# Kernel optimization log

Measured on AMD Instinct MI355X. Metric: run time of the kernel, lower is better.

Reference implementation:

```python
import jax, jax.numpy as jnp
import numpy as np

B, T, E, H = 2, 1024, 1024, 16
HD = E // H
TEMP = 0.5


def setup_inputs() -> dict:
    key = jax.random.key(0)
    ks = jax.random.split(key, 20)
    d = {
        "query1": jax.random.normal(ks[0], (B, T, E), jnp.float32),
        "query2": jax.random.normal(ks[1], (B, T, E), jnp.float32),
        "key": jax.random.normal(ks[2], (B, T, E), jnp.float32),
        "value": jax.random.normal(ks[3], (B, T, E), jnp.float32),
    }
    s = 1.0 / np.sqrt(E)
    names = ["Wq", "Wq2", "Wq3", "Wk", "Wv", "Wo"]
    for i, n in enumerate(names):
        d[n] = jax.random.normal(ks[4 + i], (E, E), jnp.float32) * s
        d["b" + n[1:]] = jax.random.normal(ks[10 + i], (E,), jnp.float32) * 0.01
    return d


def _heads(x):
    # [B,T,E] -> [B,H,T,HD]
    b, t, _ = x.shape
    return x.reshape(b, t, H, HD).transpose(0, 2, 1, 3)


def reference(query1, query2, key, value,
              Wq, bq, Wq2, bq2, Wq3, bq3, Wk, bk, Wv, bv, Wo, bo):
    q = _heads(query1 @ Wq.T + bq)
    q2 = _heads(query2 @ Wq2.T + bq2)
    q3 = _heads(key @ Wq3.T + bq3)
    k = _heads(key @ Wk.T + bk)
    v = _heads(value @ Wv.T + bv)
    b, _, t, _ = q.shape
    scale = 1.0 / np.sqrt(HD)

    def global_attn(qx):
        s = jnp.einsum('bhtd,bhsd->bhts', qx, k) * scale  # [B,H,T,T]
        # global softmax over flattened T*T, temperature-scaled, times T
        a = jax.nn.softmax((s / TEMP).reshape(b, H, t * t), axis=-1)
        return a.reshape(b, H, t, t) * t

    a1 = global_attn(q)
    a2 = global_attn(q2)
    a3 = global_attn(q3)
    attn_out = jnp.einsum('bhts,bhsd->bthd', (a1 + a2 + a3) / 3.0, v)
    attn_out = attn_out.reshape(b, t, E)
    output = attn_out @ Wo.T + bo
    return output, a1
```

## Files before the change

kernel.cpp:

```cpp
#include <hip/hip_runtime.h>
#include <hip/hip_bf16.h>


#define B_ 2
#define T_ 1024
#define E_ 1024
#define H_ 16
#define HD_ 64
#define BH_ 32

#define CEXP 0.36067376022224085f

typedef float f32x4 __attribute__((ext_vector_type(4)));
typedef short bfrag __attribute__((ext_vector_type(8)));

__device__ __forceinline__ unsigned short f2b(float f) {
  unsigned int u = __float_as_uint(f);
  u += 0x7fffu + ((u >> 16) & 1u);
  return (unsigned short)(u >> 16);
}

__device__ __forceinline__ float fexp2(float x) {
  float r;
  asm("v_exp_f32 %0, %1" : "=v"(r) : "v"(x));
  return r;
}

__device__ __forceinline__ void gl_lds16(const unsigned short* g, unsigned short* l) {
  __builtin_amdgcn_global_load_lds(
      reinterpret_cast<const __attribute__((address_space(1))) unsigned int*>(
          reinterpret_cast<uintptr_t>(g)),
      reinterpret_cast<__attribute__((address_space(3))) unsigned int*>(
          reinterpret_cast<uintptr_t>(l)),
      16, 0, 0);
}

struct CvtArgs { const float* src[10]; unsigned short* dst[10]; int n[10]; };

__global__ __launch_bounds__(256) void cvt_kernel(CvtArgs a) {
  const int z = blockIdx.y;
  const float* __restrict__ s = a.src[z];
  unsigned short* __restrict__ d = a.dst[z];
  const int n = a.n[z];
  const int stride = gridDim.x * 256 * 4;
  for (int i = (blockIdx.x * 256 + threadIdx.x) * 4; i < n; i += stride) {
    float4 v = *(const float4*)(s + i);
    ushort4 o;
    o.x = f2b(v.x); o.y = f2b(v.y); o.z = f2b(v.z); o.w = f2b(v.w);
    if (z == 9) {
      const int row = i >> 10, k = i & 1023;
      *(ushort4*)(d + (size_t)row * 2048 + k) = o;
      *(ushort4*)(d + (size_t)row * 2048 + 1024 + k) = o;
    } else {
      *(ushort4*)(d + i) = o;
    }
  }
}

template <int KLEN>
__device__ __forceinline__ void mm128_core(const unsigned short* __restrict__ A,
                                           const unsigned short* __restrict__ W,
                                           int m0, int n0,
                                           unsigned short* As, unsigned short* Bs,
                                           f32x4 acc[4][4]) {
  const int tid  = threadIdx.x;
  const int lane = tid & 63, w = tid >> 6;
  const int lrow = lane & 15, quad = lane >> 4;
  const int wm = (w >> 1) * 64, wn = (w & 1) * 64;
  const int srow = tid >> 2, soff = (tid & 3) * 8;

  const unsigned short* Ar0 = A + (size_t)(m0 + srow) * KLEN + soff;
  const unsigned short* Ar1 = Ar0 + (size_t)64 * KLEN;
  const unsigned short* Br0 = W + (size_t)(n0 + srow) * KLEN + soff;
  const unsigned short* Br1 = Br0 + (size_t)64 * KLEN;
  unsigned short* Ad0 = As + tid * 8;
  unsigned short* Ad1 = As + 2048 + tid * 8;
  unsigned short* Bd0 = Bs + tid * 8;
  unsigned short* Bd1 = Bs + 2048 + tid * 8;

  for (int k0 = 0; k0 < KLEN; k0 += 32) {
    __syncthreads();
    gl_lds16(Ar0 + k0, Ad0);
    gl_lds16(Ar1 + k0, Ad1);
    gl_lds16(Br0 + k0, Bd0);
    gl_lds16(Br1 + k0, Bd1);
    __syncthreads();
    bfrag af[4], bf_[4];
#pragma unroll
    for (int mt = 0; mt < 4; mt++)
      af[mt] = *(const bfrag*)(As + (wm + mt * 16 + lrow) * 32 + quad * 8);
#pragma unroll
    for (int nt = 0; nt < 4; nt++)
      bf_[nt] = *(const bfrag*)(Bs + (wn + nt * 16 + lrow) * 32 + quad * 8);
#pragma unroll
    for (int mt = 0; mt < 4; mt++)
#pragma unroll
      for (int nt = 0; nt < 4; nt++)
        acc[mt][nt] = __builtin_amdgcn_mfma_f32_16x16x32_bf16(af[mt], bf_[nt], acc[mt][nt], 0, 0, 0);
  }
}

struct ProjArgs {
  const unsigned short* X[5];
  const unsigned short* W[5];
  const float* bias[5];
  unsigned short* dst[5];
};

__global__ __launch_bounds__(256) void proj_kernel(ProjArgs pa) {
  __shared__ unsigned short As[128 * 32];
  __shared__ unsigned short Bs[128 * 32];
  const int z = blockIdx.z;
  const int m0 = blockIdx.y * 128, n0 = blockIdx.x * 128;
  f32x4 acc[4][4];
#pragma unroll
  for (int mt = 0; mt < 4; mt++)
#pragma unroll
    for (int nt = 0; nt < 4; nt++) acc[mt][nt] = (f32x4)0.f;

  mm128_core<E_>(pa.X[z], pa.W[z], m0, n0, As, Bs, acc);

  const int tid = threadIdx.x, lane = tid & 63, w = tid >> 6;
  const int lrow = lane & 15, quad = lane >> 4;
  const int wm = (w >> 1) * 64, wn = (w & 1) * 64;
  const float* __restrict__ bias = pa.bias[z];
  unsigned short* __restrict__ dst = pa.dst[z];
  float bv[4];
#pragma unroll
  for (int nt = 0; nt < 4; nt++) bv[nt] = bias[n0 + wn + nt * 16 + lrow];
#pragma unroll
  for (int mt = 0; mt < 4; mt++)
#pragma unroll
    for (int nt = 0; nt < 4; nt++)
#pragma unroll
      for (int ii = 0; ii < 4; ii++) {
        const int m = m0 + wm + mt * 16 + quad * 4 + ii;
        const int n = n0 + wn + nt * 16 + lrow;
        const float v = acc[mt][nt][ii] + bv[nt];
        const int b = m >> 10, t = m & 1023, h = n >> 6, dd = n & 63;
        size_t idx;
        if (z == 4)
          idx = ((size_t)((b * H_ + h) * HD_ + dd)) * T_ + t;
        else
          idx = ((size_t)((b * H_ + h) * T_ + t)) * HD_ + dd;
        dst[idx] = f2b(v);
      }
}

__global__ __launch_bounds__(256) void attn_sums_kernel(
    const unsigned short* __restrict__ Q1, const unsigned short* __restrict__ Q2,
    const unsigned short* __restrict__ Q3, const unsigned short* __restrict__ Kh,
    float* __restrict__ sums) {
  const int flat = blockIdx.x + 8 * (blockIdx.y + 2 * blockIdx.z);
  const int swz  = (flat & 7) * 64 + (flat >> 3);
  const int bx   = swz & 7;
  const int shalf = (swz >> 3) & 1;
  const int bh   = swz >> 4;

  const int tid = threadIdx.x, lane = tid & 63, w = tid >> 6;
  const int lrow = lane & 15, quad = lane >> 4;
  const int tw = w >> 1, sw = w & 1;
  const int tb = bx * 128 + tw * 64;
  const int sbase = shalf * 512;
  const size_t base = (size_t)bh * T_ * HD_;
  const unsigned short* Qs[3] = {Q1 + base, Q2 + base, Q3 + base};
  const unsigned short* Kb = Kh + base;

  float ls[3][4];
#pragma unroll
  for (int i = 0; i < 3; i++)
#pragma unroll
    for (int ii = 0; ii < 4; ii++) ls[i][ii] = 0.f;

  for (int j = 0; j < 4; j++) {
    const int sb = sbase + j * 128 + sw * 64;
#pragma unroll
    for (int i = 0; i < 3; i++) {
      f32x4 acc[4][4];
#pragma unroll
      for (int mt = 0; mt < 4; mt++)
#pragma unroll
        for (int nt = 0; nt < 4; nt++) acc[mt][nt] = (f32x4)0.f;
#pragma unroll
      for (int kk = 0; kk < 2; kk++) {
        bfrag af[4], bf_[4];
#pragma unroll
        for (int mt = 0; mt < 4; mt++)
          af[mt] = *(const bfrag*)(Qs[i] + (size_t)(tb + mt * 16 + lrow) * HD_ + kk * 32 + quad * 8);
#pragma unroll
        for (int nt = 0; nt < 4; nt++)
          bf_[nt] = *(const bfrag*)(Kb + (size_t)(sb + nt * 16 + lrow) * HD_ + kk * 32 + quad * 8);
#pragma unroll
        for (int mt = 0; mt < 4; mt++)
#pragma unroll
          for (int nt = 0; nt < 4; nt++)
            acc[mt][nt] = __builtin_amdgcn_mfma_f32_16x16x32_bf16(af[mt], bf_[nt], acc[mt][nt], 0, 0, 0);
      }
#pragma unroll
      for (int mt = 0; mt < 4; mt++)
#pragma unroll
        for (int nt = 0; nt < 4; nt++)
#pragma unroll
          for (int ii = 0; ii < 4; ii++)
            ls[i][ii] += fexp2(acc[mt][nt][ii] * CEXP);
    }
  }
#pragma unroll
  for (int i = 0; i < 3; i++) {
    float v = (ls[i][0] + ls[i][1]) + (ls[i][2] + ls[i][3]);
    for (int off = 32; off > 0; off >>= 1) v += __shfl_down(v, off, 64);
    if (lane == 0) atomicAdd(&sums[i * BH_ + bh], v);
  }
}

__global__ __launch_bounds__(256) void attn_main_kernel(
    const unsigned short* __restrict__ Q1, const unsigned short* __restrict__ Q2,
    const unsigned short* __restrict__ Q3, const unsigned short* __restrict__ Kh,
    const unsigned short* __restrict__ Vt, const float* __restrict__ sums,
    float* __restrict__ a1out, unsigned short* __restrict__ attn2) {
  __shared__ unsigned short P[128 * 136];
  const int flat = blockIdx.x + 8 * (blockIdx.y + 2 * blockIdx.z);
  const int swz  = (flat & 7) * 64 + (flat >> 3);
  const int bx   = swz & 7;
  const int sh   = (swz >> 3) & 1;
  const int bh   = swz >> 4;

  const int tid = threadIdx.x, lane = tid & 63, w = tid >> 6;
  const int lrow = lane & 15, quad = lane >> 4;
  const int tw = w >> 1, sw = w & 1, dw = sw;
  const int b = bh >> 4, h = bh & 15;
  const int tb = bx * 128 + tw * 64;
  const size_t base = (size_t)bh * T_ * HD_;
  const unsigned short* Qs[3] = {Q1 + base, Q2 + base, Q3 + base};
  const unsigned short* Kb = Kh + base;
  const unsigned short* Vb = Vt + (size_t)bh * HD_ * T_;

  float r[3];
#pragma unroll
  for (int i = 0; i < 3; i++) r[i] = (float)T_ / (3.f * sums[i * BH_ + bh]);
  const float a1s = 3.f * r[0];

  f32x4 oacc[4][2];
#pragma unroll
  for (int mt = 0; mt < 4; mt++) { oacc[mt][0] = (f32x4)0.f; oacc[mt][1] = (f32x4)0.f; }

  for (int s0 = sh * 512; s0 < sh * 512 + 512; s0 += 128) {
    const int sb = s0 + sw * 64;
    f32x4 pc[4][4];
#pragma unroll
    for (int mt = 0; mt < 4; mt++)
#pragma unroll
      for (int nt = 0; nt < 4; nt++) pc[mt][nt] = (f32x4)0.f;

#pragma unroll
    for (int i = 0; i < 3; i++) {
      f32x4 acc[4][4];
#pragma unroll
      for (int mt = 0; mt < 4; mt++)
#pragma unroll
        for (int nt = 0; nt < 4; nt++) acc[mt][nt] = (f32x4)0.f;
#pragma unroll
      for (int kk = 0; kk < 2; kk++) {
        bfrag af[4], bf_[4];
#pragma unroll
        for (int mt = 0; mt < 4; mt++)
          af[mt] = *(const bfrag*)(Qs[i] + (size_t)(tb + mt * 16 + lrow) * HD_ + kk * 32 + quad * 8);
#pragma unroll
        for (int nt = 0; nt < 4; nt++)
          bf_[nt] = *(const bfrag*)(Kb + (size_t)(sb + nt * 16 + lrow) * HD_ + kk * 32 + quad * 8);
#pragma unroll
        for (int mt = 0; mt < 4; mt++)
#pragma unroll
          for (int nt = 0; nt < 4; nt++)
            acc[mt][nt] = __builtin_amdgcn_mfma_f32_16x16x32_bf16(af[mt], bf_[nt], acc[mt][nt], 0, 0, 0);
      }
      const float ri = r[i];
#pragma unroll
      for (int mt = 0; mt < 4; mt++)
#pragma unroll
        for (int nt = 0; nt < 4; nt++)
#pragma unroll
          for (int ii = 0; ii < 4; ii++) {
            const float e = fexp2(acc[mt][nt][ii] * CEXP);
            pc[mt][nt][ii] += ri * e;
            if (i == 0) {
              const int t = tb + mt * 16 + quad * 4 + ii;
              const int s = sb + nt * 16 + lrow;
              __builtin_nontemporal_store(e * a1s,
                  a1out + ((size_t)bh * T_ + t) * T_ + s);
            }
          }
    }
    __syncthreads();
#pragma unroll
    for (int mt = 0; mt < 4; mt++)
#pragma unroll
      for (int nt = 0; nt < 4; nt++)
#pragma unroll
        for (int ii = 0; ii < 4; ii++) {
          const int tl = tw * 64 + mt * 16 + quad * 4 + ii;
          const int sl = sw * 64 + nt * 16 + lrow;
          P[tl * 136 + sl] = f2b(pc[mt][nt][ii]);
        }
    __syncthreads();
#pragma unroll
    for (int kk = 0; kk < 4; kk++) {
      bfrag pf[4], vf[2];
#pragma unroll
      for (int mt = 0; mt < 4; mt++)
        pf[mt] = *(const bfrag*)(P + (tw * 64 + mt * 16 + lrow) * 136 + kk * 32 + quad * 8);
#pragma unroll
      for (int nt = 0; nt < 2; nt++)
        vf[nt] = *(const bfrag*)(Vb + (size_t)(dw * 32 + nt * 16 + lrow) * T_ + s0 + kk * 32 + quad * 8);
#pragma unroll
      for (int mt = 0; mt < 4; mt++)
#pragma unroll
        for (int nt = 0; nt < 2; nt++)
          oacc[mt][nt] = __builtin_amdgcn_mfma_f32_16x16x32_bf16(pf[mt], vf[nt], oacc[mt][nt], 0, 0, 0);
    }
  }
#pragma unroll
  for (int mt = 0; mt < 4; mt++)
#pragma unroll
    for (int nt = 0; nt < 2; nt++)
#pragma unroll
      for (int ii = 0; ii < 4; ii++) {
        const int t = tb + mt * 16 + quad * 4 + ii;
        const int dd = dw * 32 + nt * 16 + lrow;
        attn2[((size_t)(b * T_ + t)) * 2048 + sh * 1024 + h * HD_ + dd] =
            f2b(oacc[mt][nt][ii]);
      }
}

__global__ __launch_bounds__(256) void outproj_kernel(
    const unsigned short* __restrict__ A2, const unsigned short* __restrict__ W2,
    const float* __restrict__ bias, float* __restrict__ out) {
  __shared__ unsigned short As[128 * 32];
  __shared__ unsigned short Bs[128 * 32];
  const int m0 = blockIdx.y * 128, n0 = blockIdx.x * 128;
  f32x4 acc[4][4];
#pragma unroll
  for (int mt = 0; mt < 4; mt++)
#pragma unroll
    for (int nt = 0; nt < 4; nt++) acc[mt][nt] = (f32x4)0.f;

  mm128_core<2048>(A2, W2, m0, n0, As, Bs, acc);

  const int tid = threadIdx.x, lane = tid & 63, w = tid >> 6;
  const int lrow = lane & 15, quad = lane >> 4;
  const int wm = (w >> 1) * 64, wn = (w & 1) * 64;
  float bv[4];
#pragma unroll
  for (int nt = 0; nt < 4; nt++) bv[nt] = bias[n0 + wn + nt * 16 + lrow];
#pragma unroll
  for (int mt = 0; mt < 4; mt++)
#pragma unroll
    for (int nt = 0; nt < 4; nt++)
#pragma unroll
      for (int ii = 0; ii < 4; ii++) {
        const int m = m0 + wm + mt * 16 + quad * 4 + ii;
        const int n = n0 + wn + nt * 16 + lrow;
        out[(size_t)m * E_ + n] = acc[mt][nt][ii] + bv[nt];
      }
}

extern "C" void kernel_launch(void* const* d_in, const int* in_sizes, int n_in,
                              void* d_out, int out_size, void* d_ws, size_t ws_size,
                              hipStream_t stream) {
  const float* q1f  = (const float*)d_in[0];
  const float* q2f  = (const float*)d_in[1];
  const float* keyf = (const float*)d_in[2];
  const float* valf = (const float*)d_in[3];
  const float* Wq  = (const float*)d_in[4];  const float* bq  = (const float*)d_in[5];
  const float* Wq2 = (const float*)d_in[6];  const float* bq2 = (const float*)d_in[7];
  const float* Wq3 = (const float*)d_in[8];  const float* bq3 = (const float*)d_in[9];
  const float* Wk  = (const float*)d_in[10]; const float* bk  = (const float*)d_in[11];
  const float* Wv  = (const float*)d_in[12]; const float* bv  = (const float*)d_in[13];
  const float* Wo  = (const float*)d_in[14]; const float* bo  = (const float*)d_in[15];

  char* ws = (char*)d_ws;
  const size_t MB = 1024 * 1024;
  unsigned short* xq1  = (unsigned short*)(ws + 0 * MB);
  unsigned short* xq2  = (unsigned short*)(ws + 4 * MB);
  unsigned short* xkey = (unsigned short*)(ws + 8 * MB);
  unsigned short* xval = (unsigned short*)(ws + 12 * MB);
  unsigned short* wq   = (unsigned short*)(ws + 16 * MB);
  unsigned short* wq2  = (unsigned short*)(ws + 18 * MB);
  unsigned short* wq3  = (unsigned short*)(ws + 20 * MB);
  unsigned short* wk   = (unsigned short*)(ws + 22 * MB);
  unsigned short* wv   = (unsigned short*)(ws + 24 * MB);
  unsigned short* Qh1  = (unsigned short*)(ws + 28 * MB);
  unsigned short* Qh2  = (unsigned short*)(ws + 32 * MB);
  unsigned short* Qh3  = (unsigned short*)(ws + 36 * MB);
  unsigned short* Kh   = (unsigned short*)(ws + 40 * MB);
  unsigned short* Vt   = (unsigned short*)(ws + 44 * MB);
  unsigned short* attn2 = (unsigned short*)(ws + 48 * MB);
  unsigned short* wo2   = (unsigned short*)(ws + 56 * MB);
  float* sums           = (float*)(ws + 60 * MB);

  CvtArgs ca;
  const float* srcs[10] = {q1f, q2f, keyf, valf, Wq, Wq2, Wq3, Wk, Wv, Wo};
  unsigned short* dsts[10] = {xq1, xq2, xkey, xval, wq, wq2, wq3, wk, wv, wo2};
  for (int i = 0; i < 10; i++) { ca.src[i] = srcs[i]; ca.dst[i] = dsts[i]; ca.n[i] = (i < 4) ? 2097152 : 1048576; }
  cvt_kernel<<<dim3(2048, 10), 256, 0, stream>>>(ca);

  hipMemsetAsync(sums, 0, 3 * BH_ * sizeof(float), stream);

  ProjArgs pa;
  const unsigned short* Xs[5] = {xq1, xq2, xkey, xkey, xval};
  const unsigned short* Ws_[5] = {wq, wq2, wq3, wk, wv};
  const float* Bi[5] = {bq, bq2, bq3, bk, bv};
  unsigned short* Ds[5] = {Qh1, Qh2, Qh3, Kh, Vt};
  for (int i = 0; i < 5; i++) { pa.X[i] = Xs[i]; pa.W[i] = Ws_[i]; pa.bias[i] = Bi[i]; pa.dst[i] = Ds[i]; }
  proj_kernel<<<dim3(8, 16, 5), 256, 0, stream>>>(pa);

  attn_sums_kernel<<<dim3(8, 2, BH_), 256, 0, stream>>>(Qh1, Qh2, Qh3, Kh, sums);

  float* out = (float*)d_out;
  attn_main_kernel<<<dim3(8, 2, BH_), 256, 0, stream>>>(Qh1, Qh2, Qh3, Kh, Vt, sums,
                                                        out + 2097152, attn2);

  outproj_kernel<<<dim3(8, 16), 256, 0, stream>>>(attn2, wo2, bo, out);
}
```

Before: 391.2 us.

## Split attention main kernel per query branch, add combine kernel, reuse Q fragments

The attention main kernel now launches one block per query branch (3x grid) over the full key range instead of per key half. Each block computes one branch's probabilities and writes a partial output, and a new combine kernel sums the three bf16 partials. The out-projection then runs with K=1024 instead of the duplicated 2048 layout. The sums kernel splits keys into quarters, hoists Q fragments out of the key loop, and both kernels get occupancy launch bounds. This trades an extra pass over the partial outputs and an extra bf16 rounding for more parallelism and smaller per-block register state.

```diff
diff --git a/kernel.cpp b/kernel.cpp
--- a/kernel.cpp
+++ b/kernel.cpp
@@ -18,6 +18,10 @@
   unsigned int u = __float_as_uint(f);
   u += 0x7fffu + ((u >> 16) & 1u);
   return (unsigned short)(u >> 16);
+}
+
+__device__ __forceinline__ float b2f(unsigned short u) {
+  return __uint_as_float((unsigned int)u << 16);
 }
 
 __device__ __forceinline__ float fexp2(float x) {
@@ -47,13 +51,7 @@
     float4 v = *(const float4*)(s + i);
     ushort4 o;
     o.x = f2b(v.x); o.y = f2b(v.y); o.z = f2b(v.z); o.w = f2b(v.w);
-    if (z == 9) {
-      const int row = i >> 10, k = i & 1023;
-      *(ushort4*)(d + (size_t)row * 2048 + k) = o;
-      *(ushort4*)(d + (size_t)row * 2048 + 1024 + k) = o;
-    } else {
-      *(ushort4*)(d + i) = o;
-    }
+    *(ushort4*)(d + i) = o;
   }
 }
 
@@ -147,35 +145,40 @@
       }
 }
 
-__global__ __launch_bounds__(256) void attn_sums_kernel(
+__global__ __launch_bounds__(256, 4) void attn_sums_kernel(
     const unsigned short* __restrict__ Q1, const unsigned short* __restrict__ Q2,
     const unsigned short* __restrict__ Q3, const unsigned short* __restrict__ Kh,
     float* __restrict__ sums) {
-  const int flat = blockIdx.x + 8 * (blockIdx.y + 2 * blockIdx.z);
-  const int swz  = (flat & 7) * 64 + (flat >> 3);
+  const int flat = blockIdx.x + 8 * (blockIdx.y + 4 * blockIdx.z);
+  const int swz  = (flat & 7) * 128 + (flat >> 3);
   const int bx   = swz & 7;
-  const int shalf = (swz >> 3) & 1;
-  const int bh   = swz >> 4;
+  const int sy   = (swz >> 3) & 3;
+  const int bh   = swz >> 5;
 
   const int tid = threadIdx.x, lane = tid & 63, w = tid >> 6;
   const int lrow = lane & 15, quad = lane >> 4;
   const int tw = w >> 1, sw = w & 1;
   const int tb = bx * 128 + tw * 64;
-  const int sbase = shalf * 512;
+  const int sbase = sy * 256;
   const size_t base = (size_t)bh * T_ * HD_;
   const unsigned short* Qs[3] = {Q1 + base, Q2 + base, Q3 + base};
   const unsigned short* Kb = Kh + base;
 
-  float ls[3][4];
-#pragma unroll
-  for (int i = 0; i < 3; i++)
-#pragma unroll
-    for (int ii = 0; ii < 4; ii++) ls[i][ii] = 0.f;
-
-  for (int j = 0; j < 4; j++) {
-    const int sb = sbase + j * 128 + sw * 64;
-#pragma unroll
-    for (int i = 0; i < 3; i++) {
+  float ls[3][2];
+#pragma unroll
+  for (int i = 0; i < 3; i++) { ls[i][0] = 0.f; ls[i][1] = 0.f; }
+
+#pragma unroll
+  for (int i = 0; i < 3; i++) {
+    bfrag qf[2][4];
+#pragma unroll
+    for (int kk = 0; kk < 2; kk++)
+#pragma unroll
+      for (int mt = 0; mt < 4; mt++)
+        qf[kk][mt] = *(const bfrag*)(Qs[i] + (size_t)(tb + mt * 16 + lrow) * HD_ + kk * 32 + quad * 8);
+#pragma unroll
+    for (int j = 0; j < 2; j++) {
+      const int sb = sbase + j * 128 + sw * 64;
       f32x4 acc[4][4];
 #pragma unroll
       for (int mt = 0; mt < 4; mt++)
@@ -183,10 +186,7 @@
         for (int nt = 0; nt < 4; nt++) acc[mt][nt] = (f32x4)0.f;
 #pragma unroll
       for (int kk = 0; kk < 2; kk++) {
-        bfrag af[4], bf_[4];
-#pragma unroll
-        for (int mt = 0; mt < 4; mt++)
-          af[mt] = *(const bfrag*)(Qs[i] + (size_t)(tb + mt * 16 + lrow) * HD_ + kk * 32 + quad * 8);
+        bfrag bf_[4];
 #pragma unroll
         for (int nt = 0; nt < 4; nt++)
           bf_[nt] = *(const bfrag*)(Kb + (size_t)(sb + nt * 16 + lrow) * HD_ + kk * 32 + quad * 8);
@@ -194,7 +194,7 @@
         for (int mt = 0; mt < 4; mt++)
 #pragma unroll
           for (int nt = 0; nt < 4; nt++)
-            acc[mt][nt] = __builtin_amdgcn_mfma_f32_16x16x32_bf16(af[mt], bf_[nt], acc[mt][nt], 0, 0, 0);
+            acc[mt][nt] = __builtin_amdgcn_mfma_f32_16x16x32_bf16(qf[kk][mt], bf_[nt], acc[mt][nt], 0, 0, 0);
       }
 #pragma unroll
       for (int mt = 0; mt < 4; mt++)
@@ -202,28 +202,29 @@
         for (int nt = 0; nt < 4; nt++)
 #pragma unroll
           for (int ii = 0; ii < 4; ii++)
-            ls[i][ii] += fexp2(acc[mt][nt][ii] * CEXP);
+            ls[i][ii & 1] += fexp2(acc[mt][nt][ii] * CEXP);
     }
   }
 #pragma unroll
   for (int i = 0; i < 3; i++) {
-    float v = (ls[i][0] + ls[i][1]) + (ls[i][2] + ls[i][3]);
+    float v = ls[i][0] + ls[i][1];
     for (int off = 32; off > 0; off >>= 1) v += __shfl_down(v, off, 64);
     if (lane == 0) atomicAdd(&sums[i * BH_ + bh], v);
   }
 }
 
-__global__ __launch_bounds__(256) void attn_main_kernel(
+__global__ __launch_bounds__(256, 3) void attn_main_kernel(
     const unsigned short* __restrict__ Q1, const unsigned short* __restrict__ Q2,
     const unsigned short* __restrict__ Q3, const unsigned short* __restrict__ Kh,
     const unsigned short* __restrict__ Vt, const float* __restrict__ sums,
-    float* __restrict__ a1out, unsigned short* __restrict__ attn2) {
+    float* __restrict__ a1out, unsigned short* __restrict__ attnP) {
   __shared__ unsigned short P[128 * 136];
-  const int flat = blockIdx.x + 8 * (blockIdx.y + 2 * blockIdx.z);
-  const int swz  = (flat & 7) * 64 + (flat >> 3);
-  const int bx   = swz & 7;
-  const int sh   = (swz >> 3) & 1;
-  const int bh   = swz >> 4;
+  const int flat = blockIdx.x + 8 * (blockIdx.y + 3 * blockIdx.z);
+  const int swz  = (flat & 7) * 96 + (flat >> 3);
+  const int bh   = swz / 24;
+  const int rem  = swz % 24;
+  const int iq   = rem >> 3;
+  const int bx   = rem & 7;
 
   const int tid = threadIdx.x, lane = tid & 63, w = tid >> 6;
   const int lrow = lane & 15, quad = lane >> 4;
@@ -231,65 +232,43 @@
   const int b = bh >> 4, h = bh & 15;
   const int tb = bx * 128 + tw * 64;
   const size_t base = (size_t)bh * T_ * HD_;
-  const unsigned short* Qs[3] = {Q1 + base, Q2 + base, Q3 + base};
+  const unsigned short* Qb = (iq == 0 ? Q1 : (iq == 1 ? Q2 : Q3)) + base;
   const unsigned short* Kb = Kh + base;
   const unsigned short* Vb = Vt + (size_t)bh * HD_ * T_;
-
-  float r[3];
-#pragma unroll
-  for (int i = 0; i < 3; i++) r[i] = (float)T_ / (3.f * sums[i * BH_ + bh]);
-  const float a1s = 3.f * r[0];
+  unsigned short* __restrict__ dst = attnP + (size_t)iq * (2048 * 1024);
+
+  const float r = (float)T_ / (3.f * sums[iq * BH_ + bh]);
+  const float a1s = 3.f * r;
+
+  bfrag qf[2][4];
+#pragma unroll
+  for (int kk = 0; kk < 2; kk++)
+#pragma unroll
+    for (int mt = 0; mt < 4; mt++)
+      qf[kk][mt] = *(const bfrag*)(Qb + (size_t)(tb + mt * 16 + lrow) * HD_ + kk * 32 + quad * 8);
 
   f32x4 oacc[4][2];
 #pragma unroll
   for (int mt = 0; mt < 4; mt++) { oacc[mt][0] = (f32x4)0.f; oacc[mt][1] = (f32x4)0.f; }
 
-  for (int s0 = sh * 512; s0 < sh * 512 + 512; s0 += 128) {
+  for (int s0 = 0; s0 < T_; s0 += 128) {
     const int sb = s0 + sw * 64;
-    f32x4 pc[4][4];
+    f32x4 acc[4][4];
 #pragma unroll
     for (int mt = 0; mt < 4; mt++)
 #pragma unroll
-      for (int nt = 0; nt < 4; nt++) pc[mt][nt] = (f32x4)0.f;
-
-#pragma unroll
-    for (int i = 0; i < 3; i++) {
-      f32x4 acc[4][4];
-#pragma unroll
-      for (int mt = 0; mt < 4; mt++)
-#pragma unroll
-        for (int nt = 0; nt < 4; nt++) acc[mt][nt] = (f32x4)0.f;
-#pragma unroll
-      for (int kk = 0; kk < 2; kk++) {
-        bfrag af[4], bf_[4];
-#pragma unroll
-        for (int mt = 0; mt < 4; mt++)
-          af[mt] = *(const bfrag*)(Qs[i] + (size_t)(tb + mt * 16 + lrow) * HD_ + kk * 32 + quad * 8);
+      for (int nt = 0; nt < 4; nt++) acc[mt][nt] = (f32x4)0.f;
+#pragma unroll
+    for (int kk = 0; kk < 2; kk++) {
+      bfrag bf_[4];
+#pragma unroll
+      for (int nt = 0; nt < 4; nt++)
+        bf_[nt] = *(const bfrag*)(Kb + (size_t)(sb + nt * 16 + lrow) * HD_ + kk * 32 + quad * 8);
+#pragma unroll
+      for (int mt = 0; mt < 4; mt++)
 #pragma unroll
         for (int nt = 0; nt < 4; nt++)
-          bf_[nt] = *(const bfrag*)(Kb + (size_t)(sb + nt * 16 + lrow) * HD_ + kk * 32 + quad * 8);
-#pragma unroll
-        for (int mt = 0; mt < 4; mt++)
-#pragma unroll
-          for (int nt = 0; nt < 4; nt++)
-            acc[mt][nt] = __builtin_amdgcn_mfma_f32_16x16x32_bf16(af[mt], bf_[nt], acc[mt][nt], 0, 0, 0);
-      }
-      const float ri = r[i];
-#pragma unroll
-      for (int mt = 0; mt < 4; mt++)
-#pragma unroll
-        for (int nt = 0; nt < 4; nt++)
-#pragma unroll
-          for (int ii = 0; ii < 4; ii++) {
-            const float e = fexp2(acc[mt][nt][ii] * CEXP);
-            pc[mt][nt][ii] += ri * e;
-            if (i == 0) {
-              const int t = tb + mt * 16 + quad * 4 + ii;
-              const int s = sb + nt * 16 + lrow;
-              __builtin_nontemporal_store(e * a1s,
-                  a1out + ((size_t)bh * T_ + t) * T_ + s);
-            }
-          }
+          acc[mt][nt] = __builtin_amdgcn_mfma_f32_16x16x32_bf16(qf[kk][mt], bf_[nt], acc[mt][nt], 0, 0, 0);
     }
     __syncthreads();
 #pragma unroll
@@ -298,9 +277,14 @@
       for (int nt = 0; nt < 4; nt++)
 #pragma unroll
         for (int ii = 0; ii < 4; ii++) {
+          const float e = fexp2(acc[mt][nt][ii] * CEXP);
           const int tl = tw * 64 + mt * 16 + quad * 4 + ii;
           const int sl = sw * 64 + nt * 16 + lrow;
-          P[tl * 136 + sl] = f2b(pc[mt][nt][ii]);
+          P[tl * 136 + sl] = f2b(r * e);
+          if (iq == 0) {
+            __builtin_nontemporal_store(e * a1s,
+                a1out + ((size_t)bh * T_ + (tb - tw * 64 + tl)) * T_ + s0 + sl);
+          }
         }
     __syncthreads();
 #pragma unroll
@@ -327,13 +311,29 @@
       for (int ii = 0; ii < 4; ii++) {
         const int t = tb + mt * 16 + quad * 4 + ii;
         const int dd = dw * 32 + nt * 16 + lrow;
-        attn2[((size_t)(b * T_ + t)) * 2048 + sh * 1024 + h * HD_ + dd] =
-            f2b(oacc[mt][nt][ii]);
+        dst[((size_t)(b * T_ + t)) * E_ + h * HD_ + dd] = f2b(oacc[mt][nt][ii]);
       }
 }
 
+__global__ __launch_bounds__(256) void combine_kernel(
+    const unsigned short* __restrict__ p0, const unsigned short* __restrict__ p1,
+    const unsigned short* __restrict__ p2, unsigned short* __restrict__ dstc) {
+  const size_t i = ((size_t)blockIdx.x * 256 + threadIdx.x) * 8;
+  bfrag a = *(const bfrag*)(p0 + i);
+  bfrag b = *(const bfrag*)(p1 + i);
+  bfrag c = *(const bfrag*)(p2 + i);
+  bfrag o;
+#pragma unroll
+  for (int j = 0; j < 8; j++) {
+    const float f = b2f((unsigned short)a[j]) + b2f((unsigned short)b[j]) +
+                    b2f((unsigned short)c[j]);
+    o[j] = (short)f2b(f);
+  }
+  *(bfrag*)(dstc + i) = o;
+}
+
 __global__ __launch_bounds__(256) void outproj_kernel(
-    const unsigned short* __restrict__ A2, const unsigned short* __restrict__ W2,
+    const unsigned short* __restrict__ Ab, const unsigned short* __restrict__ Wb,
     const float* __restrict__ bias, float* __restrict__ out) {
   __shared__ unsigned short As[128 * 32];
   __shared__ unsigned short Bs[128 * 32];
@@ -344,7 +344,7 @@
 #pragma unroll
     for (int nt = 0; nt < 4; nt++) acc[mt][nt] = (f32x4)0.f;
 
-  mm128_core<2048>(A2, W2, m0, n0, As, Bs, acc);
+  mm128_core<E_>(Ab, Wb, m0, n0, As, Bs, acc);
 
   const int tid = threadIdx.x, lane = tid & 63, w = tid >> 6;
   const int lrow = lane & 15, quad = lane >> 4;
@@ -389,18 +389,19 @@
   unsigned short* wq3  = (unsigned short*)(ws + 20 * MB);
   unsigned short* wk   = (unsigned short*)(ws + 22 * MB);
   unsigned short* wv   = (unsigned short*)(ws + 24 * MB);
+  unsigned short* wo   = (unsigned short*)(ws + 26 * MB);
   unsigned short* Qh1  = (unsigned short*)(ws + 28 * MB);
   unsigned short* Qh2  = (unsigned short*)(ws + 32 * MB);
   unsigned short* Qh3  = (unsigned short*)(ws + 36 * MB);
   unsigned short* Kh   = (unsigned short*)(ws + 40 * MB);
   unsigned short* Vt   = (unsigned short*)(ws + 44 * MB);
-  unsigned short* attn2 = (unsigned short*)(ws + 48 * MB);
-  unsigned short* wo2   = (unsigned short*)(ws + 56 * MB);
-  float* sums           = (float*)(ws + 60 * MB);
+  unsigned short* attnP = (unsigned short*)(ws + 48 * MB);
+  unsigned short* attn  = (unsigned short*)(ws + 60 * MB);
+  float* sums           = (float*)(ws + 64 * MB);
 
   CvtArgs ca;
   const float* srcs[10] = {q1f, q2f, keyf, valf, Wq, Wq2, Wq3, Wk, Wv, Wo};
-  unsigned short* dsts[10] = {xq1, xq2, xkey, xval, wq, wq2, wq3, wk, wv, wo2};
+  unsigned short* dsts[10] = {xq1, xq2, xkey, xval, wq, wq2, wq3, wk, wv, wo};
   for (int i = 0; i < 10; i++) { ca.src[i] = srcs[i]; ca.dst[i] = dsts[i]; ca.n[i] = (i < 4) ? 2097152 : 1048576; }
   cvt_kernel<<<dim3(2048, 10), 256, 0, stream>>>(ca);
 
@@ -414,11 +415,14 @@
   for (int i = 0; i < 5; i++) { pa.X[i] = Xs[i]; pa.W[i] = Ws_[i]; pa.bias[i] = Bi[i]; pa.dst[i] = Ds[i]; }
   proj_kernel<<<dim3(8, 16, 5), 256, 0, stream>>>(pa);
 
-  attn_sums_kernel<<<dim3(8, 2, BH_), 256, 0, stream>>>(Qh1, Qh2, Qh3, Kh, sums);
+  attn_sums_kernel<<<dim3(8, 4, BH_), 256, 0, stream>>>(Qh1, Qh2, Qh3, Kh, sums);
 
   float* out = (float*)d_out;
-  attn_main_kernel<<<dim3(8, 2, BH_), 256, 0, stream>>>(Qh1, Qh2, Qh3, Kh, Vt, sums,
-                                                        out + 2097152, attn2);
-
-  outproj_kernel<<<dim3(8, 16), 256, 0, stream>>>(attn2, wo2, bo, out);
-}
+  attn_main_kernel<<<dim3(8, 3, BH_), 256, 0, stream>>>(Qh1, Qh2, Qh3, Kh, Vt, sums,
+                                                        out + 2097152, attnP);
+
+  combine_kernel<<<dim3(1024), 256, 0, stream>>>(attnP, attnP + 4 * MB / 2,
+                                                 attnP + 8 * MB / 2, attn);
+
+  outproj_kernel<<<dim3(8, 16), 256, 0, stream>>>(attn, wo, bo, out);
+}
```

Result: slower. 602.7 us (+54.1%).
